# Kernel optimization log

Measured on AMD Instinct MI355X. Metric: run time of the kernel, lower is better.

Reference implementation:

```python
import jax, jax.numpy as jnp
import numpy as np

H = 4            # attention heads (HGTConv and SGFormer)
HID = 128        # hidden_dim
D = HID // H     # per-head dim in HGT
OUT = 128        # out_dim
L = 2            # number of HGT layers
NE, NA = 60000, 30000
E_EE, E_EA, E_AE = 150000, 75000, 75000


def setup_inputs() -> dict:
    ks = iter(jax.random.split(jax.random.key(0), 64))

    def nrm(shape, s=0.05):
        return jax.random.normal(next(ks), shape, dtype=jnp.float32) * s

    return {
        "x_entity": nrm((NE, HID), 1.0),
        "x_attr": nrm((NA, HID), 1.0),
        "Wkqv_ent": nrm((L, HID, 3 * HID)), "bkqv_ent": jnp.zeros((L, 3 * HID), jnp.float32),
        "Wkqv_att": nrm((L, HID, 3 * HID)), "bkqv_att": jnp.zeros((L, 3 * HID), jnp.float32),
        "Wout_ent": nrm((L, HID, HID)), "bout_ent": jnp.zeros((L, HID), jnp.float32),
        "Wout_att": nrm((L, HID, HID)), "bout_att": jnp.zeros((L, HID), jnp.float32),
        "skip_ent": jnp.ones((L,), jnp.float32), "skip_att": jnp.ones((L,), jnp.float32),
        "a_rel": nrm((L, 3, H, D, D), 0.1), "m_rel": nrm((L, 3, H, D, D), 0.1),
        "p_rel": jnp.ones((L, 3, H), jnp.float32),
        "ln_ent_g": jnp.ones((HID,), jnp.float32), "ln_ent_b": jnp.zeros((HID,), jnp.float32),
        "sg_fc_W": nrm((HID, HID)), "sg_fc_b": jnp.zeros((HID,), jnp.float32),
        "sg_ln0_g": jnp.ones((HID,), jnp.float32), "sg_ln0_b": jnp.zeros((HID,), jnp.float32),
        "sg_Wq": nrm((HID, HID * H)), "sg_bq": jnp.zeros((HID * H,), jnp.float32),
        "sg_Wk": nrm((HID, HID * H)), "sg_bk": jnp.zeros((HID * H,), jnp.float32),
        "sg_Wv": nrm((HID, HID * H)), "sg_bv": jnp.zeros((HID * H,), jnp.float32),
        "sg_ln1_g": jnp.ones((HID,), jnp.float32), "sg_ln1_b": jnp.zeros((HID,), jnp.float32),
        "proj_W1": nrm((HID, OUT)), "proj_b1": jnp.zeros((OUT,), jnp.float32),
        "proj_W2": nrm((OUT, OUT)), "proj_b2": jnp.zeros((OUT,), jnp.float32),
        "ei_ee": jax.random.randint(next(ks), (2, E_EE), 0, NE),
        "ei_ea": jnp.stack([jax.random.randint(next(ks), (E_EA,), 0, NE),
                            jax.random.randint(next(ks), (E_EA,), 0, NA)]),
        "ei_ae": jnp.stack([jax.random.randint(next(ks), (E_AE,), 0, NA),
                            jax.random.randint(next(ks), (E_AE,), 0, NE)]),
    }


def _ln(x, g, b, eps=1e-5):
    mu = x.mean(-1, keepdims=True)
    var = ((x - mu) ** 2).mean(-1, keepdims=True)
    return (x - mu) * jax.lax.rsqrt(var + eps) * g + b


def _seg_softmax(alpha, idx, n):
    # numerically stable softmax over edges grouped by destination node
    m = jax.ops.segment_max(alpha, idx, num_segments=n)
    e = jnp.exp(alpha - m[idx])
    s = jax.ops.segment_sum(e, idx, num_segments=n)
    return e / (s[idx] + 1e-16)


def _hgt_layer(x_e, x_a, Wkqv_e, bkqv_e, Wkqv_a, bkqv_a, Wout_e, bout_e,
               Wout_a, bout_a, sk_e, sk_a, a_rel, m_rel, p_rel,
               ei_ee, ei_ea, ei_ae):
    ne, na = x_e.shape[0], x_a.shape[0]
    # HeteroDictLinear producing [k|q|v], split along channels then reshape [N,H,D]
    kqv_e = (x_e @ Wkqv_e + bkqv_e).reshape(ne, 3, H, D)
    kqv_a = (x_a @ Wkqv_a + bkqv_a).reshape(na, 3, H, D)
    kd = {"e": kqv_e[:, 0], "a": kqv_a[:, 0]}
    qd = {"e": kqv_e[:, 1], "a": kqv_a[:, 1]}
    vd = {"e": kqv_e[:, 2], "a": kqv_a[:, 2]}
    nd = {"e": ne, "a": na}
    scale = 1.0 / float(np.sqrt(D))
    buf = {"e": [], "a": []}
    for t, (src, dst, ei) in enumerate([("e", "e", ei_ee), ("e", "a", ei_ea), ("a", "e", ei_ae)]):
        kt = jnp.einsum('nhd,hde->nhe', kd[src], a_rel[t])  # per-relation key transform (k_rel)
        vt = jnp.einsum('nhd,hde->nhe', vd[src], m_rel[t])  # per-relation value transform (v_rel)
        al = (qd[dst][ei[1]] * kt[ei[0]]).sum(-1) * p_rel[t] * scale  # [E,H]
        buf[dst].append((al, vt[ei[0]], ei[1]))
    outs = {}
    for dst in ("e", "a"):
        # joint softmax over ALL incoming edge types of this node type
        al = jnp.concatenate([b[0] for b in buf[dst]], 0)
        ve = jnp.concatenate([b[1] for b in buf[dst]], 0)
        ix = jnp.concatenate([b[2] for b in buf[dst]], 0)
        w = _seg_softmax(al, ix, nd[dst])
        outs[dst] = jax.ops.segment_sum(ve * w[..., None], ix,
                                        num_segments=nd[dst]).reshape(nd[dst], HID)
    o_e = jax.nn.gelu(outs["e"], approximate=False) @ Wout_e + bout_e
    o_a = jax.nn.gelu(outs["a"], approximate=False) @ Wout_a + bout_a
    g_e, g_a = jax.nn.sigmoid(sk_e), jax.nn.sigmoid(sk_a)
    return g_e * o_e + (1.0 - g_e) * x_e, g_a * o_a + (1.0 - g_a) * x_a


def reference(x_entity, x_attr, Wkqv_ent, bkqv_ent, Wkqv_att, bkqv_att,
              Wout_ent, bout_ent, Wout_att, bout_att, skip_ent, skip_att,
              a_rel, m_rel, p_rel, ln_ent_g, ln_ent_b,
              sg_fc_W, sg_fc_b, sg_ln0_g, sg_ln0_b, sg_Wq, sg_bq, sg_Wk, sg_bk,
              sg_Wv, sg_bv, sg_ln1_g, sg_ln1_b,
              proj_W1, proj_b1, proj_W2, proj_b2, ei_ee, ei_ea, ei_ae):
    h_e, h_a = x_entity, x_attr
    for l in range(L):
        h_e, h_a = _hgt_layer(h_e, h_a, Wkqv_ent[l], bkqv_ent[l], Wkqv_att[l], bkqv_att[l],
                              Wout_ent[l], bout_ent[l], Wout_att[l], bout_att[l],
                              skip_ent[l], skip_att[l], a_rel[l], m_rel[l], p_rel[l],
                              ei_ee, ei_ea, ei_ae)
        h_e = jax.nn.gelu(h_e, approximate=False)
        h_a = jax.nn.gelu(h_a, approximate=False)
    # SGFormer trans_conv: fc -> LN -> ReLU -> linear global attention -> residual -> LN
    n = h_e.shape[0]
    z0 = jax.nn.relu(_ln(h_e @ sg_fc_W + sg_fc_b, sg_ln0_g, sg_ln0_b))
    q = (z0 @ sg_Wq + sg_bq).reshape(n, H, HID)
    k = (z0 @ sg_Wk + sg_bk).reshape(n, H, HID)
    v = (z0 @ sg_Wv + sg_bv).reshape(n, H, HID)
    qs = q / jnp.linalg.norm(q)  # global Frobenius norm, as in SGFormer
    kn = k / jnp.linalg.norm(k)
    kvs = jnp.einsum('lhm,lhd->hmd', kn, v)
    num = jnp.einsum('nhm,hmd->nhd', qs, kvs) + float(n) * v
    den = jnp.einsum('nhm,hm->nh', qs, kn.sum(0))[..., None] + float(n)
    attn = (num / den).mean(1)  # mean over heads -> [n, HID]
    h_global = _ln(0.5 * attn + 0.5 * z0, sg_ln1_g, sg_ln1_b)  # residual alpha=0.5
    # alpha-blend (self.alpha = 0.1) + entity LayerNorm + projector MLP
    h_ent = _ln(0.9 * h_e + 0.1 * h_global, ln_ent_g, ln_ent_b)
    return jax.nn.relu(h_ent @ proj_W1 + proj_b1) @ proj_W2 + proj_b2
```

## Files before the change

### kernel.cpp

```cpp
#include <hip/hip_runtime.h>

#define NE 60000
#define NA 30000
#define E_EE 150000
#define E_EA 75000
#define E_AE 75000
#define SCALE 0.17677669529663689f

typedef __attribute__((ext_vector_type(8))) short bf16x8;
typedef __attribute__((ext_vector_type(4))) float f32x4;

__device__ __forceinline__ float bf2f(unsigned short u) {
  return __uint_as_float(((unsigned)u) << 16);
}
__device__ __forceinline__ unsigned short f2bf(float f) {
  unsigned u = __float_as_uint(f);
  u = u + 0x7FFFu + ((u >> 16) & 1u);
  return (unsigned short)(u >> 16);
}
__device__ __forceinline__ float ldc(const float* p) { return *p; }
__device__ __forceinline__ float ldc(const unsigned short* p) { return bf2f(*p); }
__device__ __forceinline__ float gelu_f(float x) {
  return 0.5f * x * (1.0f + erff(x * 0.7071067811865476f));
}

__global__ __launch_bounds__(256) void wrel_k(
    const float* __restrict__ Wk_e, const float* __restrict__ Wk_a,
    const float* __restrict__ bk_e, const float* __restrict__ bk_a,
    const float* __restrict__ a_rel, const float* __restrict__ m_rel,
    float* __restrict__ Wkt, float* __restrict__ Wvt,
    float* __restrict__ bkt, float* __restrict__ bvt) {
  int t = blockIdx.x;
  int part = blockIdx.y;
  const float* W = (t < 2) ? Wk_e : Wk_a;
  const float* bb = (t < 2) ? bk_e : bk_a;
  const float* A = (part ? m_rel : a_rel) + t * 4096;
  int coff = part ? 256 : 0;
  float* Wo = (part ? Wvt : Wkt) + t * 16384;
  float* bo = (part ? bvt : bkt) + t * 128;
  __shared__ float As[4096];
  for (int u = threadIdx.x; u < 4096; u += 256) As[u] = A[u];
  __syncthreads();
  for (int u = threadIdx.x; u < 16384; u += 256) {
    int i = u >> 7, c = u & 127;
    int hh = c >> 5, e = c & 31;
    const float* wr = W + i * 384 + coff + hh * 32;
    const float* ar = As + hh * 1024 + e;
    float acc = 0.f;
#pragma unroll
    for (int d = 0; d < 32; ++d) acc = fmaf(wr[d], ar[d * 32], acc);
    Wo[u] = acc;
  }
  if (threadIdx.x < 128) {
    int c = threadIdx.x, hh = c >> 5, e = c & 31;
    const float* br = bb + coff + hh * 32;
    const float* ar = As + hh * 1024 + e;
    float acc = 0.f;
#pragma unroll
    for (int d = 0; d < 32; ++d) acc = fmaf(br[d], ar[d * 32], acc);
    bo[c] = acc;
  }
}

template <int ACT, int EPI>
__global__ __launch_bounds__(256) void gemm128_k(
    const float* __restrict__ X, int ldx,
    const float* __restrict__ W, int ldw,
    const float* __restrict__ bias, int N,
    float* __restrict__ fout, unsigned short* __restrict__ bout, int ldo,
    const float* __restrict__ skipp, float* __restrict__ ssq) {
  __shared__ float Xs[128 * 32];
  __shared__ float Ws[32 * 128];
  const int tid = threadIdx.x;
  const int ti = tid >> 4;
  const int tj = tid & 15;
  const int row0 = blockIdx.x * 128;
  const int cb = blockIdx.y * 128;
  const int c0 = cb + tj * 4;
  const int c1 = cb + 64 + tj * 4;

  float acc[8][8];
  {
    float bc[8] = {0.f, 0.f, 0.f, 0.f, 0.f, 0.f, 0.f, 0.f};
    if (bias) {
#pragma unroll
      for (int j = 0; j < 4; ++j) { bc[j] = bias[c0 + j]; bc[4 + j] = bias[c1 + j]; }
    }
#pragma unroll
    for (int i = 0; i < 8; ++i)
#pragma unroll
      for (int j = 0; j < 8; ++j) acc[i][j] = bc[j];
  }

  for (int ks = 0; ks < 128; ks += 32) {
    __syncthreads();
    for (int v = tid; v < 1024; v += 256) {
      int kq = v & 7, r = v >> 3;
      int rg = row0 + r; if (rg >= N) rg = N - 1;
      float4 x4 = *reinterpret_cast<const float4*>(X + (size_t)rg * ldx + ks + kq * 4);
      if (ACT == 1) {
        x4.x = gelu_f(x4.x); x4.y = gelu_f(x4.y);
        x4.z = gelu_f(x4.z); x4.w = gelu_f(x4.w);
      }
      *reinterpret_cast<float4*>(&Xs[r * 32 + ((kq ^ ((r >> 3) & 7)) << 2)]) = x4;
    }
    for (int v = tid; v < 1024; v += 256) {
      int cq = v & 31, k = v >> 5;
      *reinterpret_cast<float4*>(&Ws[k * 128 + cq * 4]) =
          *reinterpret_cast<const float4*>(W + (size_t)(ks + k) * ldw + cb + cq * 4);
    }
    __syncthreads();
#pragma unroll
    for (int k = 0; k < 32; k += 4) {
      float xr[8][4];
#pragma unroll
      for (int i = 0; i < 8; ++i)
        *reinterpret_cast<float4*>(xr[i]) = *reinterpret_cast<const float4*>(
            &Xs[(ti * 8 + i) * 32 + ((((k >> 2)) ^ (ti & 7)) << 2)]);
      float wr[4][8];
#pragma unroll
      for (int dk = 0; dk < 4; ++dk) {
        *reinterpret_cast<float4*>(&wr[dk][0]) =
            *reinterpret_cast<const float4*>(&Ws[(k + dk) * 128 + tj * 4]);
        *reinterpret_cast<float4*>(&wr[dk][4]) =
            *reinterpret_cast<const float4*>(&Ws[(k + dk) * 128 + 64 + tj * 4]);
      }
#pragma unroll
      for (int i = 0; i < 8; ++i)
#pragma unroll
        for (int dk = 0; dk < 4; ++dk)
#pragma unroll
          for (int j = 0; j < 8; ++j)
            acc[i][j] = fmaf(xr[i][dk], wr[dk][j], acc[i][j]);
    }
  }

  if (EPI == 0 || EPI == 1) {
#pragma unroll
    for (int i = 0; i < 8; ++i) {
      int rg = row0 + ti * 8 + i;
      if (rg < N) {
        float4 a = make_float4(acc[i][0], acc[i][1], acc[i][2], acc[i][3]);
        float4 b = make_float4(acc[i][4], acc[i][5], acc[i][6], acc[i][7]);
        if (EPI == 1) {
          a.x = fmaxf(a.x, 0.f); a.y = fmaxf(a.y, 0.f);
          a.z = fmaxf(a.z, 0.f); a.w = fmaxf(a.w, 0.f);
          b.x = fmaxf(b.x, 0.f); b.y = fmaxf(b.y, 0.f);
          b.z = fmaxf(b.z, 0.f); b.w = fmaxf(b.w, 0.f);
        }
        *reinterpret_cast<float4*>(fout + (size_t)rg * ldo + c0) = a;
        *reinterpret_cast<float4*>(fout + (size_t)rg * ldo + c1) = b;
      }
    }
  } else if (EPI == 2) {
    float loc = 0.f;
#pragma unroll
    for (int i = 0; i < 8; ++i) {
      int rg = row0 + ti * 8 + i;
      if (rg < N) {
        ushort4 s0, s1;
        s0.x = f2bf(acc[i][0]); s0.y = f2bf(acc[i][1]);
        s0.z = f2bf(acc[i][2]); s0.w = f2bf(acc[i][3]);
        s1.x = f2bf(acc[i][4]); s1.y = f2bf(acc[i][5]);
        s1.z = f2bf(acc[i][6]); s1.w = f2bf(acc[i][7]);
        *reinterpret_cast<ushort4*>(bout + (size_t)rg * ldo + c0) = s0;
        *reinterpret_cast<ushort4*>(bout + (size_t)rg * ldo + c1) = s1;
#pragma unroll
        for (int j = 0; j < 8; ++j) loc += acc[i][j] * acc[i][j];
      }
    }
    if (ssq) {
      __syncthreads();
      Xs[tid] = loc;
      __syncthreads();
      if (tid < 128) Xs[tid] += Xs[tid + 128];
      __syncthreads();
      if (tid < 64) {
        float v = Xs[tid] + Xs[tid + 64];
#pragma unroll
        for (int m = 32; m > 0; m >>= 1) v += __shfl_down(v, m, 64);
        if (tid == 0) atomicAdd(ssq, v);
      }
    }
  } else {
    float g = 1.f / (1.f + expf(-*skipp));
    float g1 = 1.f - g;
#pragma unroll
    for (int i = 0; i < 8; ++i) {
      int rg = row0 + ti * 8 + i;
      if (rg < N) {
        float4 o0 = *reinterpret_cast<const float4*>(fout + (size_t)rg * ldo + c0);
        float4 o1 = *reinterpret_cast<const float4*>(fout + (size_t)rg * ldo + c1);
        float4 a, b;
        a.x = gelu_f(g * acc[i][0] + g1 * o0.x);
        a.y = gelu_f(g * acc[i][1] + g1 * o0.y);
        a.z = gelu_f(g * acc[i][2] + g1 * o0.z);
        a.w = gelu_f(g * acc[i][3] + g1 * o0.w);
        b.x = gelu_f(g * acc[i][4] + g1 * o1.x);
        b.y = gelu_f(g * acc[i][5] + g1 * o1.y);
        b.z = gelu_f(g * acc[i][6] + g1 * o1.z);
        b.w = gelu_f(g * acc[i][7] + g1 * o1.w);
        *reinterpret_cast<float4*>(fout + (size_t)rg * ldo + c0) = a;
        *reinterpret_cast<float4*>(fout + (size_t)rg * ldo + c1) = b;
      }
    }
  }
}

template <int ACT, int EPI>
__global__ __launch_bounds__(256) void gemm64_k(
    const float* __restrict__ X, int ldx,
    const float* __restrict__ W, int ldw,
    const float* __restrict__ bias, int N,
    float* __restrict__ fout, unsigned short* __restrict__ bout, int ldo,
    const float* __restrict__ skipp, float* __restrict__ ssq) {
  __shared__ float Xs[64 * 32];
  __shared__ float Ws[32 * 128];
  const int tid = threadIdx.x;
  const int ti = tid >> 4;
  const int tj = tid & 15;
  const int row0 = blockIdx.x * 64;
  const int cb = blockIdx.y * 128;
  const int c0 = cb + tj * 4;
  const int c1 = cb + 64 + tj * 4;

  float acc[4][8];
  {
    float bc[8] = {0.f, 0.f, 0.f, 0.f, 0.f, 0.f, 0.f, 0.f};
    if (bias) {
#pragma unroll
      for (int j = 0; j < 4; ++j) { bc[j] = bias[c0 + j]; bc[4 + j] = bias[c1 + j]; }
    }
#pragma unroll
    for (int i = 0; i < 4; ++i)
#pragma unroll
      for (int j = 0; j < 8; ++j) acc[i][j] = bc[j];
  }

  for (int ks = 0; ks < 128; ks += 32) {
    __syncthreads();
    for (int v = tid; v < 512; v += 256) {
      int kq = v & 7, r = v >> 3;
      int rg = row0 + r; if (rg >= N) rg = N - 1;
      float4 x4 = *reinterpret_cast<const float4*>(X + (size_t)rg * ldx + ks + kq * 4);
      if (ACT == 1) {
        x4.x = gelu_f(x4.x); x4.y = gelu_f(x4.y);
        x4.z = gelu_f(x4.z); x4.w = gelu_f(x4.w);
      }
      *reinterpret_cast<float4*>(&Xs[r * 32 + ((kq ^ ((r >> 3) & 7)) << 2)]) = x4;
    }
    for (int v = tid; v < 1024; v += 256) {
      int cq = v & 31, k = v >> 5;
      *reinterpret_cast<float4*>(&Ws[k * 128 + cq * 4]) =
          *reinterpret_cast<const float4*>(W + (size_t)(ks + k) * ldw + cb + cq * 4);
    }
    __syncthreads();
#pragma unroll
    for (int k = 0; k < 32; k += 4) {
      float xr[4][4];
#pragma unroll
      for (int i = 0; i < 4; ++i)
        *reinterpret_cast<float4*>(xr[i]) = *reinterpret_cast<const float4*>(
            &Xs[(ti * 4 + i) * 32 + ((((k >> 2)) ^ (ti >> 1)) << 2)]);
      float wr[4][8];
#pragma unroll
      for (int dk = 0; dk < 4; ++dk) {
        *reinterpret_cast<float4*>(&wr[dk][0]) =
            *reinterpret_cast<const float4*>(&Ws[(k + dk) * 128 + tj * 4]);
        *reinterpret_cast<float4*>(&wr[dk][4]) =
            *reinterpret_cast<const float4*>(&Ws[(k + dk) * 128 + 64 + tj * 4]);
      }
#pragma unroll
      for (int i = 0; i < 4; ++i)
#pragma unroll
        for (int dk = 0; dk < 4; ++dk)
#pragma unroll
          for (int j = 0; j < 8; ++j)
            acc[i][j] = fmaf(xr[i][dk], wr[dk][j], acc[i][j]);
    }
  }

  if (EPI == 0 || EPI == 1) {
#pragma unroll
    for (int i = 0; i < 4; ++i) {
      int rg = row0 + ti * 4 + i;
      if (rg < N) {
        float4 a = make_float4(acc[i][0], acc[i][1], acc[i][2], acc[i][3]);
        float4 b = make_float4(acc[i][4], acc[i][5], acc[i][6], acc[i][7]);
        if (EPI == 1) {
          a.x = fmaxf(a.x, 0.f); a.y = fmaxf(a.y, 0.f);
          a.z = fmaxf(a.z, 0.f); a.w = fmaxf(a.w, 0.f);
          b.x = fmaxf(b.x, 0.f); b.y = fmaxf(b.y, 0.f);
          b.z = fmaxf(b.z, 0.f); b.w = fmaxf(b.w, 0.f);
        }
        *reinterpret_cast<float4*>(fout + (size_t)rg * ldo + c0) = a;
        *reinterpret_cast<float4*>(fout + (size_t)rg * ldo + c1) = b;
      }
    }
  } else if (EPI == 2) {
    float loc = 0.f;
#pragma unroll
    for (int i = 0; i < 4; ++i) {
      int rg = row0 + ti * 4 + i;
      if (rg < N) {
        ushort4 s0, s1;
        s0.x = f2bf(acc[i][0]); s0.y = f2bf(acc[i][1]);
        s0.z = f2bf(acc[i][2]); s0.w = f2bf(acc[i][3]);
        s1.x = f2bf(acc[i][4]); s1.y = f2bf(acc[i][5]);
        s1.z = f2bf(acc[i][6]); s1.w = f2bf(acc[i][7]);
        *reinterpret_cast<ushort4*>(bout + (size_t)rg * ldo + c0) = s0;
        *reinterpret_cast<ushort4*>(bout + (size_t)rg * ldo + c1) = s1;
#pragma unroll
        for (int j = 0; j < 8; ++j) loc += acc[i][j] * acc[i][j];
      }
    }
    if (ssq) {
      __syncthreads();
      Xs[tid] = loc;
      __syncthreads();
      if (tid < 128) Xs[tid] += Xs[tid + 128];
      __syncthreads();
      if (tid < 64) {
        float v = Xs[tid] + Xs[tid + 64];
#pragma unroll
        for (int m = 32; m > 0; m >>= 1) v += __shfl_down(v, m, 64);
        if (tid == 0) atomicAdd(ssq, v);
      }
    }
  } else {
    float g = 1.f / (1.f + expf(-*skipp));
    float g1 = 1.f - g;
#pragma unroll
    for (int i = 0; i < 4; ++i) {
      int rg = row0 + ti * 4 + i;
      if (rg < N) {
        float4 o0 = *reinterpret_cast<const float4*>(fout + (size_t)rg * ldo + c0);
        float4 o1 = *reinterpret_cast<const float4*>(fout + (size_t)rg * ldo + c1);
        float4 a, b;
        a.x = gelu_f(g * acc[i][0] + g1 * o0.x);
        a.y = gelu_f(g * acc[i][1] + g1 * o0.y);
        a.z = gelu_f(g * acc[i][2] + g1 * o0.z);
        a.w = gelu_f(g * acc[i][3] + g1 * o0.w);
        b.x = gelu_f(g * acc[i][4] + g1 * o1.x);
        b.y = gelu_f(g * acc[i][5] + g1 * o1.y);
        b.z = gelu_f(g * acc[i][6] + g1 * o1.z);
        b.w = gelu_f(g * acc[i][7] + g1 * o1.w);
        *reinterpret_cast<float4*>(fout + (size_t)rg * ldo + c0) = a;
        *reinterpret_cast<float4*>(fout + (size_t)rg * ldo + c1) = b;
      }
    }
  }
}

template <int EPI>
__global__ __launch_bounds__(256) void gemmMF_k(
    const float* __restrict__ X, int ldx,
    const float* __restrict__ W, int ldw,
    const float* __restrict__ bias, int N,
    float* __restrict__ fout, unsigned short* __restrict__ bout, int ldo,
    float* __restrict__ ssq) {
  __shared__ short Bs[16384];
  const int tid = threadIdx.x;
  const int lane = tid & 63;
  const int w = tid >> 6;
  const int n0 = blockIdx.x * 64;
  const int cb = blockIdx.y * 128;

  for (int s = tid; s < 2048; s += 256) {
    int l = s & 63, dtks = s >> 6;
    int c = cb + (dtks >> 2) * 16 + (l & 15);
    int kk = (dtks & 3) * 32 + (l >> 4) * 8;
    bf16x8 b;
#pragma unroll
    for (int j = 0; j < 8; ++j)
      b[j] = (short)f2bf(W[(size_t)(kk + j) * ldw + c]);
    *reinterpret_cast<bf16x8*>(&Bs[s * 8]) = b;
  }

  int arow = n0 + w * 16 + (lane & 15);
  if (arow >= N) arow = N - 1;
  const int kofs = (lane >> 4) * 8;
  bf16x8 afr[4];
#pragma unroll
  for (int ks = 0; ks < 4; ++ks) {
    const float* xp = X + (size_t)arow * ldx + ks * 32 + kofs;
    float4 a0 = *reinterpret_cast<const float4*>(xp);
    float4 a1 = *reinterpret_cast<const float4*>(xp + 4);
    bf16x8 a;
    a[0] = (short)f2bf(a0.x); a[1] = (short)f2bf(a0.y);
    a[2] = (short)f2bf(a0.z); a[3] = (short)f2bf(a0.w);
    a[4] = (short)f2bf(a1.x); a[5] = (short)f2bf(a1.y);
    a[6] = (short)f2bf(a1.z); a[7] = (short)f2bf(a1.w);
    afr[ks] = a;
  }
  __syncthreads();

  float loc = 0.f;
#pragma unroll
  for (int dt = 0; dt < 8; ++dt) {
    f32x4 acc = {0.f, 0.f, 0.f, 0.f};
#pragma unroll
    for (int ks = 0; ks < 4; ++ks) {
      bf16x8 b = *reinterpret_cast<const bf16x8*>(&Bs[((dt * 4 + ks) * 64 + lane) * 8]);
      acc = __builtin_amdgcn_mfma_f32_16x16x32_bf16(afr[ks], b, acc, 0, 0, 0);
    }
    int dcol = dt * 16 + (lane & 15);
    float bv = bias ? bias[cb + dcol] : 0.f;
#pragma unroll
    for (int r = 0; r < 4; ++r) {
      int rg = n0 + w * 16 + (lane >> 4) * 4 + r;
      if (rg < N) {
        float val = acc[r] + bv;
        if (EPI == 0) {
          fout[(size_t)rg * ldo + cb + dcol] = val;
        } else {
          bout[(size_t)rg * ldo + cb + dcol] = f2bf(val);
          loc += val * val;
        }
      }
    }
  }
  if (EPI == 2 && ssq) {
    __syncthreads();
    float* red = (float*)Bs;
    red[tid] = loc;
    __syncthreads();
    if (tid < 128) red[tid] += red[tid + 128];
    __syncthreads();
    if (tid < 64) {
      float v = red[tid] + red[tid + 64];
#pragma unroll
      for (int m = 32; m > 0; m >>= 1) v += __shfl_down(v, m, 64);
      if (tid == 0) atomicAdd(ssq, v);
    }
  }
}

__global__ __launch_bounds__(256) void deg_k(const int* __restrict__ ei, int E,
                                             int* __restrict__ deg) {
  int i = blockIdx.x * 256 + threadIdx.x;
  if (i < E) atomicAdd(&deg[ei[E + i]], 1);
}

__global__ __launch_bounds__(1024) void scan_k(int* __restrict__ deg_cursor,
                                               int* __restrict__ rowptr, int n) {
  __shared__ int sd[1024];
  __shared__ int carry;
  int tid = threadIdx.x;
  if (tid == 0) carry = 0;
  __syncthreads();
  for (int base = 0; base < n; base += 1024) {
    int v = (base + tid < n) ? deg_cursor[base + tid] : 0;
    sd[tid] = v;
    __syncthreads();
    for (int off = 1; off < 1024; off <<= 1) {
      int t = (tid >= off) ? sd[tid - off] : 0;
      __syncthreads();
      sd[tid] += t;
      __syncthreads();
    }
    int c0 = carry;
    if (base + tid < n) {
      int excl = c0 + sd[tid] - v;
      rowptr[base + tid] = excl;
      deg_cursor[base + tid] = excl;
    }
    __syncthreads();
    if (tid == 0) carry = c0 + sd[1023];
    __syncthreads();
  }
  if (tid == 0) rowptr[n] = carry;
}

__global__ __launch_bounds__(256) void fill_k(const int* __restrict__ ei, int E,
                                              int* __restrict__ cursor,
                                              int* __restrict__ entries,
                                              int srcoff, int tag) {
  int i = blockIdx.x * 256 + threadIdx.x;
  if (i < E) {
    int pos = atomicAdd(&cursor[ei[E + i]], 1);
    entries[pos] = (ei[i] + srcoff) | (tag << 30);
  }
}

__global__ __launch_bounds__(256) void hgt_gather_k(
    const float* __restrict__ q, const unsigned short* __restrict__ ktbl,
    const unsigned short* __restrict__ vtbl, const int* __restrict__ rowptr,
    const int* __restrict__ entries, const float* __restrict__ pbase, int nd,
    float* __restrict__ out) {
  int g = blockIdx.x * 8 + (threadIdx.x >> 5);
  int dst = g >> 2, h = g & 3, c = threadIdx.x & 31;
  if (dst >= nd) return;
  int col = h * 32 + c;
  float qv = q[(size_t)dst * 128 + col];
  int i0 = rowptr[dst], i1 = rowptr[dst + 1];
  float sum = 0.f, acc = 0.f;
  for (int i = i0; i < i1; ++i) {
    int e = entries[i];
    int lin = e & 0x3FFFFFFF;
    int tag = (unsigned)e >> 30;
    float part = qv * bf2f(ktbl[(size_t)lin * 128 + col]);
#pragma unroll
    for (int m = 16; m > 0; m >>= 1) part += __shfl_xor(part, m);
    float w = expf(part * SCALE * pbase[tag * 8 + h]);
    sum += w;
    acc = fmaf(w, bf2f(vtbl[(size_t)lin * 128 + col]), acc);
  }
  out[(size_t)dst * 128 + col] = acc / (sum + 1e-16f);
}

template <typename AT, typename BT>
__global__ __launch_bounds__(128) void ln_k(const AT* __restrict__ A,
                                            const BT* __restrict__ B, float alpha,
                                            float beta, const float* __restrict__ g,
                                            const float* __restrict__ b,
                                            float* __restrict__ out, int relu) {
  int row = blockIdx.x;
  int t = threadIdx.x;
  float v = alpha * ldc(A + (size_t)row * 128 + t);
  if (B) v += beta * ldc(B + (size_t)row * 128 + t);
  float s1 = v, s2 = v * v;
#pragma unroll
  for (int m = 32; m > 0; m >>= 1) {
    s1 += __shfl_xor(s1, m, 64);
    s2 += __shfl_xor(s2, m, 64);
  }
  __shared__ float r1[2], r2[2];
  int w = t >> 6;
  if ((t & 63) == 0) { r1[w] = s1; r2[w] = s2; }
  __syncthreads();
  float S1 = r1[0] + r1[1], S2 = r2[0] + r2[1];
  float mu = S1 * (1.f / 128.f);
  float var = S2 * (1.f / 128.f) - mu * mu;
  float rr = rsqrtf(fmaxf(var, 0.f) + 1e-5f);
  float o = (v - mu) * rr * g[t] + b[t];
  if (relu) o = fmaxf(o, 0.f);
  out[(size_t)row * 128 + t] = o;
}

__global__ __launch_bounds__(256) void kvsred_k(const unsigned short* __restrict__ Kb,
                                                const unsigned short* __restrict__ Vb,
                                                float* __restrict__ part,
                                                float* __restrict__ ksum, int chunk) {
  const int h = blockIdx.y;
  const int n0 = blockIdx.x * chunk;
  const int iters = chunk >> 3;
  __shared__ float ks[8][132];
  __shared__ float vs[8][132];
  const int tid = threadIdx.x;
  const int ti = tid >> 4, tj = tid & 15;

  const int sw = tid >> 7;
  const int sni = (tid >> 4) & 7;
  const int sc = (tid & 15) << 3;
  const unsigned short* src =
      (sw ? Vb : Kb) + (size_t)(n0 + sni) * 512 + h * 128 + sc;
  float* dstrow = (sw ? &vs[0][0] : &ks[0][0]) + sni * 132 + sc;

  float acc[8][8];
#pragma unroll
  for (int i = 0; i < 8; ++i)
#pragma unroll
    for (int j = 0; j < 8; ++j) acc[i][j] = 0.f;
  float ksloc = 0.f;

  uint4 r = *reinterpret_cast<const uint4*>(src);
  for (int it = 0; it < iters; ++it) {
    __syncthreads();
    float4 lo, hi;
    lo.x = bf2f((unsigned short)(r.x & 0xffffu)); lo.y = bf2f((unsigned short)(r.x >> 16));
    lo.z = bf2f((unsigned short)(r.y & 0xffffu)); lo.w = bf2f((unsigned short)(r.y >> 16));
    hi.x = bf2f((unsigned short)(r.z & 0xffffu)); hi.y = bf2f((unsigned short)(r.z >> 16));
    hi.z = bf2f((unsigned short)(r.w & 0xffffu)); hi.w = bf2f((unsigned short)(r.w >> 16));
    *reinterpret_cast<float4*>(dstrow) = lo;
    *reinterpret_cast<float4*>(dstrow + 4) = hi;
    if (it + 1 < iters)
      r = *reinterpret_cast<const uint4*>(src + (size_t)(it + 1) * 8 * 512);
    __syncthreads();
#pragma unroll
    for (int ni = 0; ni < 8; ++ni) {
      float kk[8], vv[8];
      *reinterpret_cast<float4*>(kk) =
          *reinterpret_cast<const float4*>(&ks[ni][ti * 4]);
      *reinterpret_cast<float4*>(kk + 4) =
          *reinterpret_cast<const float4*>(&ks[ni][64 + ti * 4]);
      *reinterpret_cast<float4*>(vv) =
          *reinterpret_cast<const float4*>(&vs[ni][tj * 4]);
      *reinterpret_cast<float4*>(vv + 4) =
          *reinterpret_cast<const float4*>(&vs[ni][64 + tj * 4]);
#pragma unroll
      for (int i = 0; i < 8; ++i)
#pragma unroll
        for (int j = 0; j < 8; ++j) acc[i][j] = fmaf(kk[i], vv[j], acc[i][j]);
      if (tid < 128) ksloc += ks[ni][tid];
    }
  }
  float* pb = part + (size_t)(blockIdx.x * 4 + h) * 16384;
#pragma unroll
  for (int i = 0; i < 8; ++i) {
    int m = ti * 4 + (i & 3) + ((i >> 2) << 6);
    *reinterpret_cast<float4*>(pb + m * 128 + tj * 4) =
        make_float4(acc[i][0], acc[i][1], acc[i][2], acc[i][3]);
    *reinterpret_cast<float4*>(pb + m * 128 + 64 + tj * 4) =
        make_float4(acc[i][4], acc[i][5], acc[i][6], acc[i][7]);
  }
  if (tid < 128) atomicAdd(&ksum[h * 128 + tid], ksloc);
}

__global__ __launch_bounds__(256) void kvsfin_k(const float* __restrict__ part,
                                                float* __restrict__ kvs,
                                                unsigned short* __restrict__ kvsT,
                                                int G) {
  int c = blockIdx.x * 256 + threadIdx.x;
  int hh = c >> 14, md = c & 16383;
  int m = md >> 7, d = md & 127;
  const float* p = part + (size_t)hh * 16384 + md;
  float s = 0.f;
#pragma unroll 4
  for (int g = 0; g < G; ++g) s += p[(size_t)g * 65536];
  kvs[c] = s;
  kvsT[hh * 16384 + d * 128 + m] = f2bf(s);
}

__global__ __launch_bounds__(256) void sgapply_k(const unsigned short* __restrict__ Qb,
                                                 const unsigned short* __restrict__ Vb,
                                                 const unsigned short* __restrict__ kvsT,
                                                 const float* __restrict__ ksum,
                                                 const float* __restrict__ ssqq,
                                                 const float* __restrict__ ssqk,
                                                 unsigned short* __restrict__ attnb,
                                                 int N) {
  __shared__ short Bs[16384];
  __shared__ float den_s[64];
  __shared__ float fsh_s;
  const int tid = threadIdx.x;
  const int lane = tid & 63;
  const int w = tid >> 6;
  const int n0 = blockIdx.x * 64;
  if (tid == 0) fsh_s = 1.0f / (sqrtf(*ssqq) * sqrtf(*ssqk));

  float out[8][4];
#pragma unroll
  for (int dt = 0; dt < 8; ++dt)
#pragma unroll
    for (int r = 0; r < 4; ++r) out[dt][r] = 0.f;

  int arow = n0 + w * 16 + (lane & 15);
  if (arow >= N) arow = N - 1;
  const int kofs = (lane >> 4) * 8;

  for (int h = 0; h < 4; ++h) {
    __syncthreads();
    for (int s = tid; s < 2048; s += 256) {
      int l = s & 63, dtks = s >> 6;
      int d = (dtks >> 2) * 16 + (l & 15);
      int kk = (dtks & 3) * 32 + (l >> 4) * 8;
      *reinterpret_cast<bf16x8*>(&Bs[s * 8]) =
          *reinterpret_cast<const bf16x8*>(kvsT + h * 16384 + d * 128 + kk);
    }
    {
      int r = tid >> 2, seg = tid & 3;
      int rg = n0 + r; if (rg >= N) rg = N - 1;
      const unsigned short* qp = Qb + (size_t)rg * 512 + h * 128 + seg * 32;
      const float* kp = ksum + h * 128 + seg * 32;
      float p = 0.f;
#pragma unroll
      for (int u = 0; u < 32; u += 8) {
        bf16x8 q8 = *reinterpret_cast<const bf16x8*>(qp + u);
#pragma unroll
        for (int j = 0; j < 8; ++j)
          p = fmaf(bf2f((unsigned short)q8[j]), kp[u + j], p);
      }
      p += __shfl_xor(p, 1);
      p += __shfl_xor(p, 2);
      if (seg == 0) den_s[r] = p * fsh_s + 60000.0f;
    }
    __syncthreads();
    bf16x8 afr[4];
    {
      const unsigned short* qrow = Qb + (size_t)arow * 512 + h * 128 + kofs;
#pragma unroll
      for (int ks = 0; ks < 4; ++ks)
        afr[ks] = *reinterpret_cast<const bf16x8*>(qrow + ks * 32);
    }
    float f = fsh_s;
#pragma unroll
    for (int dt = 0; dt < 8; ++dt) {
      f32x4 acc = {0.f, 0.f, 0.f, 0.f};
#pragma unroll
      for (int ks = 0; ks < 4; ++ks) {
        bf16x8 b = *reinterpret_cast<const bf16x8*>(&Bs[((dt * 4 + ks) * 64 + lane) * 8]);
        acc = __builtin_amdgcn_mfma_f32_16x16x32_bf16(afr[ks], b, acc, 0, 0, 0);
      }
      int dcol = dt * 16 + (lane & 15);
#pragma unroll
      for (int r = 0; r < 4; ++r) {
        int rl = w * 16 + (lane >> 4) * 4 + r;
        int rg = n0 + rl;
        if (rg < N) {
          float v = bf2f(Vb[(size_t)rg * 512 + h * 128 + dcol]);
          float rd = 1.0f / den_s[rl];
          out[dt][r] += (acc[r] * f + 60000.0f * v) * rd;
        }
      }
    }
  }
#pragma unroll
  for (int dt = 0; dt < 8; ++dt) {
    int dcol = dt * 16 + (lane & 15);
#pragma unroll
    for (int r = 0; r < 4; ++r) {
      int rg = n0 + w * 16 + (lane >> 4) * 4 + r;
      if (rg < N) attnb[(size_t)rg * 128 + dcol] = f2bf(0.25f * out[dt][r]);
    }
  }
}

extern "C" void kernel_launch(void* const* d_in, const int* in_sizes, int n_in,
                              void* d_out, int out_size, void* d_ws, size_t ws_size,
                              hipStream_t stream) {
  const float* x_ent = (const float*)d_in[0];
  const float* x_att = (const float*)d_in[1];
  const float* Wkqv_e = (const float*)d_in[2];
  const float* bkqv_e = (const float*)d_in[3];
  const float* Wkqv_a = (const float*)d_in[4];
  const float* bkqv_a = (const float*)d_in[5];
  const float* Wout_e = (const float*)d_in[6];
  const float* bout_e = (const float*)d_in[7];
  const float* Wout_a = (const float*)d_in[8];
  const float* bout_a = (const float*)d_in[9];
  const float* skip_e = (const float*)d_in[10];
  const float* skip_a = (const float*)d_in[11];
  const float* a_rel = (const float*)d_in[12];
  const float* m_rel = (const float*)d_in[13];
  const float* p_rel = (const float*)d_in[14];
  const float* ln_ent_g = (const float*)d_in[15];
  const float* ln_ent_b = (const float*)d_in[16];
  const float* sg_fc_W = (const float*)d_in[17];
  const float* sg_fc_b = (const float*)d_in[18];
  const float* sg_ln0_g = (const float*)d_in[19];
  const float* sg_ln0_b = (const float*)d_in[20];
  const float* sg_Wq = (const float*)d_in[21];
  const float* sg_bq = (const float*)d_in[22];
  const float* sg_Wk = (const float*)d_in[23];
  const float* sg_bk = (const float*)d_in[24];
  const float* sg_Wv = (const float*)d_in[25];
  const float* sg_bv = (const float*)d_in[26];
  const float* sg_ln1_g = (const float*)d_in[27];
  const float* sg_ln1_b = (const float*)d_in[28];
  const float* proj_W1 = (const float*)d_in[29];
  const float* proj_b1 = (const float*)d_in[30];
  const float* proj_W2 = (const float*)d_in[31];
  const float* proj_b2 = (const float*)d_in[32];
  const int* ei_ee = (const int*)d_in[33];
  const int* ei_ea = (const int*)d_in[34];
  const int* ei_ae = (const int*)d_in[35];

  char* ws = (char*)d_ws;
  const size_t O_HE = 0;
  const size_t O_HA = 30720000;
  const size_t O_Z0 = 46080000;
  const size_t O_WKT = 76800000;
  const size_t O_WVT = 76996608;
  const size_t O_BKT = 77193216;
  const size_t O_BVT = 77194752;
  const size_t O_KVS = 77196288;
  const size_t O_RPE = 77460544;
  const size_t O_RPA = O_RPE + 240064;
  const size_t O_CUE = O_RPA + 120064;
  const size_t O_CUA = O_CUE + 240000;
  const size_t O_ENE = O_CUA + 120000;
  const size_t O_ENA = O_ENE + 900000;
  const size_t O_UN = O_ENA + 300000;
  float* q_e = (float*)(ws + O_UN);
  float* q_a = (float*)(ws + O_UN + 30720000);
  unsigned short* ktbl = (unsigned short*)(ws + O_UN + 46080000);
  unsigned short* vtbl = (unsigned short*)(ws + O_UN + 84480000);
  float* tmpf = (float*)(ws + O_UN);
  unsigned short* Vb = (unsigned short*)(ws + O_UN);
  unsigned short* KQb = (unsigned short*)(ws + O_UN + 61440000);
  unsigned short* attnb = (unsigned short*)(ws + O_HA);

  float* h_e = (float*)(ws + O_HE);
  float* h_a = (float*)(ws + O_HA);
  float* z0 = (float*)(ws + O_Z0);
  float* Wkt = (float*)(ws + O_WKT);
  float* Wvt = (float*)(ws + O_WVT);
  float* bkt = (float*)(ws + O_BKT);
  float* bvt = (float*)(ws + O_BVT);
  float* kvs = (float*)(ws + O_KVS);
  float* ksum = (float*)(ws + O_KVS + 262144);
  float* ssq_q = (float*)(ws + O_KVS + 262144 + 2048);
  float* ssq_k = ssq_q + 1;
  int* rowptr_e = (int*)(ws + O_RPE);
  int* rowptr_a = (int*)(ws + O_RPA);
  int* cursor_e = (int*)(ws + O_CUE);
  int* cursor_a = (int*)(ws + O_CUA);
  int* entries_e = (int*)(ws + O_ENE);
  int* entries_a = (int*)(ws + O_ENA);

  const int GB_E = (NE + 127) / 128;
  const int G64_E = (NE + 63) / 64;
  const int G64_A = (NA + 63) / 64;

  hipMemcpyAsync(h_e, x_ent, (size_t)NE * 128 * 4, hipMemcpyDeviceToDevice, stream);
  hipMemcpyAsync(h_a, x_att, (size_t)NA * 128 * 4, hipMemcpyDeviceToDevice, stream);

  hipMemsetAsync(ws + O_CUE, 0, 360000, stream);
  deg_k<<<(E_EE + 255) / 256, 256, 0, stream>>>(ei_ee, E_EE, cursor_e);
  deg_k<<<(E_AE + 255) / 256, 256, 0, stream>>>(ei_ae, E_AE, cursor_e);
  deg_k<<<(E_EA + 255) / 256, 256, 0, stream>>>(ei_ea, E_EA, cursor_a);
  scan_k<<<1, 1024, 0, stream>>>(cursor_e, rowptr_e, NE);
  scan_k<<<1, 1024, 0, stream>>>(cursor_a, rowptr_a, NA);
  fill_k<<<(E_EE + 255) / 256, 256, 0, stream>>>(ei_ee, E_EE, cursor_e, entries_e, 0, 0);
  fill_k<<<(E_AE + 255) / 256, 256, 0, stream>>>(ei_ae, E_AE, cursor_e, entries_e, NE, 1);
  fill_k<<<(E_EA + 255) / 256, 256, 0, stream>>>(ei_ea, E_EA, cursor_a, entries_a, 0, 0);

  for (int l = 0; l < 2; ++l) {
    const float* Wke = Wkqv_e + (size_t)l * 49152;
    const float* Wka = Wkqv_a + (size_t)l * 49152;
    const float* bke = bkqv_e + (size_t)l * 384;
    const float* bka = bkqv_a + (size_t)l * 384;

    wrel_k<<<dim3(3, 2), 256, 0, stream>>>(Wke, Wka, bke, bka,
                                           a_rel + (size_t)l * 12288,
                                           m_rel + (size_t)l * 12288, Wkt, Wvt, bkt, bvt);
    gemm64_k<0, 0><<<G64_E, 256, 0, stream>>>(h_e, 128, Wke + 128, 384, bke + 128, NE,
                                              q_e, nullptr, 128, nullptr, nullptr);
    gemm64_k<0, 0><<<G64_A, 256, 0, stream>>>(h_a, 128, Wka + 128, 384, bka + 128, NA,
                                              q_a, nullptr, 128, nullptr, nullptr);
    gemm64_k<0, 2><<<G64_E, 256, 0, stream>>>(h_e, 128, Wkt, 128, bkt, NE,
                                              nullptr, ktbl, 128, nullptr, nullptr);
    gemm64_k<0, 2><<<G64_A, 256, 0, stream>>>(h_a, 128, Wkt + 2 * 16384, 128,
                                              bkt + 2 * 128, NA, nullptr,
                                              ktbl + (size_t)NE * 128, 128, nullptr, nullptr);
    gemm64_k<0, 2><<<G64_E, 256, 0, stream>>>(h_e, 128, Wkt + 1 * 16384, 128,
                                              bkt + 1 * 128, NE, nullptr,
                                              ktbl + (size_t)90000 * 128, 128, nullptr, nullptr);
    gemm64_k<0, 2><<<G64_E, 256, 0, stream>>>(h_e, 128, Wvt, 128, bvt, NE,
                                              nullptr, vtbl, 128, nullptr, nullptr);
    gemm64_k<0, 2><<<G64_A, 256, 0, stream>>>(h_a, 128, Wvt + 2 * 16384, 128,
                                              bvt + 2 * 128, NA, nullptr,
                                              vtbl + (size_t)NE * 128, 128, nullptr, nullptr);
    gemm64_k<0, 2><<<G64_E, 256, 0, stream>>>(h_e, 128, Wvt + 1 * 16384, 128,
                                              bvt + 1 * 128, NE, nullptr,
                                              vtbl + (size_t)90000 * 128, 128, nullptr, nullptr);
    hgt_gather_k<<<30000, 256, 0, stream>>>(q_e, ktbl, vtbl, rowptr_e, entries_e,
                                            p_rel + (size_t)l * 12, NE, q_e);
    hgt_gather_k<<<15000, 256, 0, stream>>>(q_a, ktbl + (size_t)90000 * 128,
                                            vtbl + (size_t)90000 * 128, rowptr_a,
                                            entries_a, p_rel + (size_t)l * 12 + 4, NA, q_a);
    gemm64_k<1, 3><<<G64_E, 256, 0, stream>>>(q_e, 128, Wout_e + (size_t)l * 16384, 128,
                                              bout_e + (size_t)l * 128, NE, h_e, nullptr,
                                              128, skip_e + l, nullptr);
    gemm64_k<1, 3><<<G64_A, 256, 0, stream>>>(q_a, 128, Wout_a + (size_t)l * 16384, 128,
                                              bout_a + (size_t)l * 128, NA, h_a, nullptr,
                                              128, skip_a + l, nullptr);
  }

  gemmMF_k<0><<<dim3(G64_E, 1), 256, 0, stream>>>(h_e, 128, sg_fc_W, 128, sg_fc_b, NE,
                                                  tmpf, nullptr, 128, nullptr);
  ln_k<float, float><<<NE, 128, 0, stream>>>(tmpf, nullptr, 1.f, 0.f, sg_ln0_g,
                                             sg_ln0_b, z0, 1);
  hipMemsetAsync(ws + O_KVS, 0, 264256, stream);
  gemmMF_k<2><<<dim3(G64_E, 4), 256, 0, stream>>>(z0, 128, sg_Wv, 512, sg_bv, NE,
                                                  nullptr, Vb, 512, nullptr);
  gemmMF_k<2><<<dim3(G64_E, 4), 256, 0, stream>>>(z0, 128, sg_Wk, 512, sg_bk, NE,
                                                  nullptr, KQb, 512, ssq_k);
  unsigned short* kvsT = (unsigned short*)((char*)d_out + 26214400);
  kvsred_k<<<dim3(100, 4), 256, 0, stream>>>(KQb, Vb, (float*)d_out, ksum, 600);
  kvsfin_k<<<256, 256, 0, stream>>>((const float*)d_out, kvs, kvsT, 100);
  gemmMF_k<2><<<dim3(G64_E, 4), 256, 0, stream>>>(z0, 128, sg_Wq, 512, sg_bq, NE,
                                                  nullptr, KQb, 512, ssq_q);
  sgapply_k<<<G64_E, 256, 0, stream>>>(KQb, Vb, kvsT, ksum, ssq_q, ssq_k, attnb, NE);
  ln_k<unsigned short, float><<<NE, 128, 0, stream>>>(attnb, z0, 0.5f, 0.5f, sg_ln1_g,
                                                      sg_ln1_b, z0, 0);
  ln_k<float, float><<<NE, 128, 0, stream>>>(h_e, z0, 0.9f, 0.1f, ln_ent_g, ln_ent_b,
                                             h_e, 0);
  gemm64_k<0, 1><<<G64_E, 256, 0, stream>>>(h_e, 128, proj_W1, 128, proj_b1, NE,
                                            z0, nullptr, 128, nullptr, nullptr);
  gemm64_k<0, 0><<<G64_E, 256, 0, stream>>>(z0, 128, proj_W2, 128, proj_b2, NE,
                                            (float*)d_out, nullptr, 128, nullptr, nullptr);
}
```

Baseline: 1.825 ms.

## Compute SGFormer K^T V reduction with bf16 MFMA and split column sums

Rewrites the K^T·V partial reduction to use bf16 MFMA 16x16x32 instructions on an LDS tile laid out for the MFMA operands, replacing the scalar FMA outer-product loop. Partial results are now stored as bf16, which halves the traffic into the final reduce. The grid grows to 188 chunks of 320 rows with bounds checks. The K column sum moves into a separate colsum kernel that uses atomics. An unused 128-row GEMM kernel is deleted. Rounding the partial sums to bf16 adds precision loss in the global reduction.

```diff
diff --git a/kernel.cpp b/kernel.cpp
--- a/kernel.cpp
+++ b/kernel.cpp
@@ -63,151 +63,6 @@
 }
 
 template <int ACT, int EPI>
-__global__ __launch_bounds__(256) void gemm128_k(
-    const float* __restrict__ X, int ldx,
-    const float* __restrict__ W, int ldw,
-    const float* __restrict__ bias, int N,
-    float* __restrict__ fout, unsigned short* __restrict__ bout, int ldo,
-    const float* __restrict__ skipp, float* __restrict__ ssq) {
-  __shared__ float Xs[128 * 32];
-  __shared__ float Ws[32 * 128];
-  const int tid = threadIdx.x;
-  const int ti = tid >> 4;
-  const int tj = tid & 15;
-  const int row0 = blockIdx.x * 128;
-  const int cb = blockIdx.y * 128;
-  const int c0 = cb + tj * 4;
-  const int c1 = cb + 64 + tj * 4;
-
-  float acc[8][8];
-  {
-    float bc[8] = {0.f, 0.f, 0.f, 0.f, 0.f, 0.f, 0.f, 0.f};
-    if (bias) {
-#pragma unroll
-      for (int j = 0; j < 4; ++j) { bc[j] = bias[c0 + j]; bc[4 + j] = bias[c1 + j]; }
-    }
-#pragma unroll
-    for (int i = 0; i < 8; ++i)
-#pragma unroll
-      for (int j = 0; j < 8; ++j) acc[i][j] = bc[j];
-  }
-
-  for (int ks = 0; ks < 128; ks += 32) {
-    __syncthreads();
-    for (int v = tid; v < 1024; v += 256) {
-      int kq = v & 7, r = v >> 3;
-      int rg = row0 + r; if (rg >= N) rg = N - 1;
-      float4 x4 = *reinterpret_cast<const float4*>(X + (size_t)rg * ldx + ks + kq * 4);
-      if (ACT == 1) {
-        x4.x = gelu_f(x4.x); x4.y = gelu_f(x4.y);
-        x4.z = gelu_f(x4.z); x4.w = gelu_f(x4.w);
-      }
-      *reinterpret_cast<float4*>(&Xs[r * 32 + ((kq ^ ((r >> 3) & 7)) << 2)]) = x4;
-    }
-    for (int v = tid; v < 1024; v += 256) {
-      int cq = v & 31, k = v >> 5;
-      *reinterpret_cast<float4*>(&Ws[k * 128 + cq * 4]) =
-          *reinterpret_cast<const float4*>(W + (size_t)(ks + k) * ldw + cb + cq * 4);
-    }
-    __syncthreads();
-#pragma unroll
-    for (int k = 0; k < 32; k += 4) {
-      float xr[8][4];
-#pragma unroll
-      for (int i = 0; i < 8; ++i)
-        *reinterpret_cast<float4*>(xr[i]) = *reinterpret_cast<const float4*>(
-            &Xs[(ti * 8 + i) * 32 + ((((k >> 2)) ^ (ti & 7)) << 2)]);
-      float wr[4][8];
-#pragma unroll
-      for (int dk = 0; dk < 4; ++dk) {
-        *reinterpret_cast<float4*>(&wr[dk][0]) =
-            *reinterpret_cast<const float4*>(&Ws[(k + dk) * 128 + tj * 4]);
-        *reinterpret_cast<float4*>(&wr[dk][4]) =
-            *reinterpret_cast<const float4*>(&Ws[(k + dk) * 128 + 64 + tj * 4]);
-      }
-#pragma unroll
-      for (int i = 0; i < 8; ++i)
-#pragma unroll
-        for (int dk = 0; dk < 4; ++dk)
-#pragma unroll
-          for (int j = 0; j < 8; ++j)
-            acc[i][j] = fmaf(xr[i][dk], wr[dk][j], acc[i][j]);
-    }
-  }
-
-  if (EPI == 0 || EPI == 1) {
-#pragma unroll
-    for (int i = 0; i < 8; ++i) {
-      int rg = row0 + ti * 8 + i;
-      if (rg < N) {
-        float4 a = make_float4(acc[i][0], acc[i][1], acc[i][2], acc[i][3]);
-        float4 b = make_float4(acc[i][4], acc[i][5], acc[i][6], acc[i][7]);
-        if (EPI == 1) {
-          a.x = fmaxf(a.x, 0.f); a.y = fmaxf(a.y, 0.f);
-          a.z = fmaxf(a.z, 0.f); a.w = fmaxf(a.w, 0.f);
-          b.x = fmaxf(b.x, 0.f); b.y = fmaxf(b.y, 0.f);
-          b.z = fmaxf(b.z, 0.f); b.w = fmaxf(b.w, 0.f);
-        }
-        *reinterpret_cast<float4*>(fout + (size_t)rg * ldo + c0) = a;
-        *reinterpret_cast<float4*>(fout + (size_t)rg * ldo + c1) = b;
-      }
-    }
-  } else if (EPI == 2) {
-    float loc = 0.f;
-#pragma unroll
-    for (int i = 0; i < 8; ++i) {
-      int rg = row0 + ti * 8 + i;
-      if (rg < N) {
-        ushort4 s0, s1;
-        s0.x = f2bf(acc[i][0]); s0.y = f2bf(acc[i][1]);
-        s0.z = f2bf(acc[i][2]); s0.w = f2bf(acc[i][3]);
-        s1.x = f2bf(acc[i][4]); s1.y = f2bf(acc[i][5]);
-        s1.z = f2bf(acc[i][6]); s1.w = f2bf(acc[i][7]);
-        *reinterpret_cast<ushort4*>(bout + (size_t)rg * ldo + c0) = s0;
-        *reinterpret_cast<ushort4*>(bout + (size_t)rg * ldo + c1) = s1;
-#pragma unroll
-        for (int j = 0; j < 8; ++j) loc += acc[i][j] * acc[i][j];
-      }
-    }
-    if (ssq) {
-      __syncthreads();
-      Xs[tid] = loc;
-      __syncthreads();
-      if (tid < 128) Xs[tid] += Xs[tid + 128];
-      __syncthreads();
-      if (tid < 64) {
-        float v = Xs[tid] + Xs[tid + 64];
-#pragma unroll
-        for (int m = 32; m > 0; m >>= 1) v += __shfl_down(v, m, 64);
-        if (tid == 0) atomicAdd(ssq, v);
-      }
-    }
-  } else {
-    float g = 1.f / (1.f + expf(-*skipp));
-    float g1 = 1.f - g;
-#pragma unroll
-    for (int i = 0; i < 8; ++i) {
-      int rg = row0 + ti * 8 + i;
-      if (rg < N) {
-        float4 o0 = *reinterpret_cast<const float4*>(fout + (size_t)rg * ldo + c0);
-        float4 o1 = *reinterpret_cast<const float4*>(fout + (size_t)rg * ldo + c1);
-        float4 a, b;
-        a.x = gelu_f(g * acc[i][0] + g1 * o0.x);
-        a.y = gelu_f(g * acc[i][1] + g1 * o0.y);
-        a.z = gelu_f(g * acc[i][2] + g1 * o0.z);
-        a.w = gelu_f(g * acc[i][3] + g1 * o0.w);
-        b.x = gelu_f(g * acc[i][4] + g1 * o1.x);
-        b.y = gelu_f(g * acc[i][5] + g1 * o1.y);
-        b.z = gelu_f(g * acc[i][6] + g1 * o1.z);
-        b.w = gelu_f(g * acc[i][7] + g1 * o1.w);
-        *reinterpret_cast<float4*>(fout + (size_t)rg * ldo + c0) = a;
-        *reinterpret_cast<float4*>(fout + (size_t)rg * ldo + c1) = b;
-      }
-    }
-  }
-}
-
-template <int ACT, int EPI>
 __global__ __launch_bounds__(256) void gemm64_k(
     const float* __restrict__ X, int ldx,
     const float* __restrict__ W, int ldw,
@@ -538,86 +393,96 @@
   out[(size_t)row * 128 + t] = o;
 }
 
+__global__ __launch_bounds__(256) void colsum_k(const unsigned short* __restrict__ Kb,
+                                                float* __restrict__ ksum, int N) {
+  int c2 = threadIdx.x * 2;
+  int r0 = blockIdx.x * 128;
+  int r1 = r0 + 128; if (r1 > N) r1 = N;
+  float s0 = 0.f, s1 = 0.f;
+  for (int r = r0; r < r1; ++r) {
+    unsigned v = *reinterpret_cast<const unsigned*>(Kb + (size_t)r * 512 + c2);
+    s0 += bf2f((unsigned short)(v & 0xffffu));
+    s1 += bf2f((unsigned short)(v >> 16));
+  }
+  atomicAdd(&ksum[c2], s0);
+  atomicAdd(&ksum[c2 + 1], s1);
+}
+
 __global__ __launch_bounds__(256) void kvsred_k(const unsigned short* __restrict__ Kb,
                                                 const unsigned short* __restrict__ Vb,
-                                                float* __restrict__ part,
-                                                float* __restrict__ ksum, int chunk) {
+                                                unsigned short* __restrict__ part16,
+                                                int chunk, int N) {
+  __shared__ short Ks[4096];
+  __shared__ short Vs[4096];
+  const int tid = threadIdx.x;
+  const int lane = tid & 63;
+  const int w = tid >> 6;
   const int h = blockIdx.y;
-  const int n0 = blockIdx.x * chunk;
-  const int iters = chunk >> 3;
-  __shared__ float ks[8][132];
-  __shared__ float vs[8][132];
-  const int tid = threadIdx.x;
-  const int ti = tid >> 4, tj = tid & 15;
-
-  const int sw = tid >> 7;
-  const int sni = (tid >> 4) & 7;
-  const int sc = (tid & 15) << 3;
-  const unsigned short* src =
-      (sw ? Vb : Kb) + (size_t)(n0 + sni) * 512 + h * 128 + sc;
-  float* dstrow = (sw ? &vs[0][0] : &ks[0][0]) + sni * 132 + sc;
-
-  float acc[8][8];
-#pragma unroll
-  for (int i = 0; i < 8; ++i)
-#pragma unroll
-    for (int j = 0; j < 8; ++j) acc[i][j] = 0.f;
-  float ksloc = 0.f;
-
-  uint4 r = *reinterpret_cast<const uint4*>(src);
-  for (int it = 0; it < iters; ++it) {
-    __syncthreads();
-    float4 lo, hi;
-    lo.x = bf2f((unsigned short)(r.x & 0xffffu)); lo.y = bf2f((unsigned short)(r.x >> 16));
-    lo.z = bf2f((unsigned short)(r.y & 0xffffu)); lo.w = bf2f((unsigned short)(r.y >> 16));
-    hi.x = bf2f((unsigned short)(r.z & 0xffffu)); hi.y = bf2f((unsigned short)(r.z >> 16));
-    hi.z = bf2f((unsigned short)(r.w & 0xffffu)); hi.w = bf2f((unsigned short)(r.w >> 16));
-    *reinterpret_cast<float4*>(dstrow) = lo;
-    *reinterpret_cast<float4*>(dstrow + 4) = hi;
-    if (it + 1 < iters)
-      r = *reinterpret_cast<const uint4*>(src + (size_t)(it + 1) * 8 * 512);
-    __syncthreads();
-#pragma unroll
-    for (int ni = 0; ni < 8; ++ni) {
-      float kk[8], vv[8];
-      *reinterpret_cast<float4*>(kk) =
-          *reinterpret_cast<const float4*>(&ks[ni][ti * 4]);
-      *reinterpret_cast<float4*>(kk + 4) =
-          *reinterpret_cast<const float4*>(&ks[ni][64 + ti * 4]);
-      *reinterpret_cast<float4*>(vv) =
-          *reinterpret_cast<const float4*>(&vs[ni][tj * 4]);
-      *reinterpret_cast<float4*>(vv + 4) =
-          *reinterpret_cast<const float4*>(&vs[ni][64 + tj * 4]);
-#pragma unroll
-      for (int i = 0; i < 8; ++i)
-#pragma unroll
-        for (int j = 0; j < 8; ++j) acc[i][j] = fmaf(kk[i], vv[j], acc[i][j]);
-      if (tid < 128) ksloc += ks[ni][tid];
-    }
-  }
-  float* pb = part + (size_t)(blockIdx.x * 4 + h) * 16384;
-#pragma unroll
-  for (int i = 0; i < 8; ++i) {
-    int m = ti * 4 + (i & 3) + ((i >> 2) << 6);
-    *reinterpret_cast<float4*>(pb + m * 128 + tj * 4) =
-        make_float4(acc[i][0], acc[i][1], acc[i][2], acc[i][3]);
-    *reinterpret_cast<float4*>(pb + m * 128 + 64 + tj * 4) =
-        make_float4(acc[i][4], acc[i][5], acc[i][6], acc[i][7]);
-  }
-  if (tid < 128) atomicAdd(&ksum[h * 128 + tid], ksloc);
-}
-
-__global__ __launch_bounds__(256) void kvsfin_k(const float* __restrict__ part,
+  const int n0b = blockIdx.x * chunk;
+
+  f32x4 acc[2][8];
+#pragma unroll
+  for (int mi = 0; mi < 2; ++mi)
+#pragma unroll
+    for (int dt = 0; dt < 8; ++dt) acc[mi][dt] = (f32x4){0.f, 0.f, 0.f, 0.f};
+
+  for (int nc = 0; nc < chunk; nc += 32) {
+    int n0 = n0b + nc;
+    __syncthreads();
+    for (int u = tid; u < 1024; u += 256) {
+      int mat = u >> 9, rem = u & 511;
+      int nr = rem >> 4, c0 = (rem & 15) << 3;
+      int n = n0 + nr;
+      uint4 val = make_uint4(0u, 0u, 0u, 0u);
+      if (n < N)
+        val = *reinterpret_cast<const uint4*>(
+            (mat ? Vb : Kb) + (size_t)n * 512 + h * 128 + c0);
+      short* dst = mat ? Vs : Ks;
+      int base = (((c0 >> 4) * 64 + (nr >> 3) * 16 + (c0 & 15)) << 3) + (nr & 7);
+      unsigned short v[8];
+      v[0] = (unsigned short)(val.x & 0xffffu); v[1] = (unsigned short)(val.x >> 16);
+      v[2] = (unsigned short)(val.y & 0xffffu); v[3] = (unsigned short)(val.y >> 16);
+      v[4] = (unsigned short)(val.z & 0xffffu); v[5] = (unsigned short)(val.z >> 16);
+      v[6] = (unsigned short)(val.w & 0xffffu); v[7] = (unsigned short)(val.w >> 16);
+#pragma unroll
+      for (int i = 0; i < 8; ++i) dst[base + (i << 3)] = (short)v[i];
+    }
+    __syncthreads();
+    bf16x8 a0 = *reinterpret_cast<const bf16x8*>(&Ks[((2 * w) * 64 + lane) * 8]);
+    bf16x8 a1 = *reinterpret_cast<const bf16x8*>(&Ks[((2 * w + 1) * 64 + lane) * 8]);
+#pragma unroll
+    for (int dt = 0; dt < 8; ++dt) {
+      bf16x8 b = *reinterpret_cast<const bf16x8*>(&Vs[(dt * 64 + lane) * 8]);
+      acc[0][dt] = __builtin_amdgcn_mfma_f32_16x16x32_bf16(a0, b, acc[0][dt], 0, 0, 0);
+      acc[1][dt] = __builtin_amdgcn_mfma_f32_16x16x32_bf16(a1, b, acc[1][dt], 0, 0, 0);
+    }
+  }
+  unsigned short* pb = part16 + (size_t)(blockIdx.x * 4 + h) * 16384;
+#pragma unroll
+  for (int mi = 0; mi < 2; ++mi) {
+    int mt = 2 * w + mi;
+#pragma unroll
+    for (int dt = 0; dt < 8; ++dt) {
+      int col = dt * 16 + (lane & 15);
+#pragma unroll
+      for (int r = 0; r < 4; ++r) {
+        int row = mt * 16 + (lane >> 4) * 4 + r;
+        pb[row * 128 + col] = f2bf(acc[mi][dt][r]);
+      }
+    }
+  }
+}
+
+__global__ __launch_bounds__(256) void kvsfin_k(const unsigned short* __restrict__ part16,
                                                 float* __restrict__ kvs,
                                                 unsigned short* __restrict__ kvsT,
                                                 int G) {
   int c = blockIdx.x * 256 + threadIdx.x;
   int hh = c >> 14, md = c & 16383;
   int m = md >> 7, d = md & 127;
-  const float* p = part + (size_t)hh * 16384 + md;
   float s = 0.f;
-#pragma unroll 4
-  for (int g = 0; g < G; ++g) s += p[(size_t)g * 65536];
+  for (int g = 0; g < G; ++g)
+    s += bf2f(part16[((size_t)g * 4 + hh) * 16384 + md]);
   kvs[c] = s;
   kvsT[hh * 16384 + d * 128 + m] = f2bf(s);
 }
@@ -799,7 +664,6 @@
   int* entries_e = (int*)(ws + O_ENE);
   int* entries_a = (int*)(ws + O_ENA);
 
-  const int GB_E = (NE + 127) / 128;
   const int G64_E = (NE + 63) / 64;
   const int G64_A = (NA + 63) / 64;
 
@@ -867,9 +731,11 @@
                                                   nullptr, Vb, 512, nullptr);
   gemmMF_k<2><<<dim3(G64_E, 4), 256, 0, stream>>>(z0, 128, sg_Wk, 512, sg_bk, NE,
                                                   nullptr, KQb, 512, ssq_k);
-  unsigned short* kvsT = (unsigned short*)((char*)d_out + 26214400);
-  kvsred_k<<<dim3(100, 4), 256, 0, stream>>>(KQb, Vb, (float*)d_out, ksum, 600);
-  kvsfin_k<<<256, 256, 0, stream>>>((const float*)d_out, kvs, kvsT, 100);
+  colsum_k<<<469, 256, 0, stream>>>(KQb, ksum, NE);
+  unsigned short* part16 = (unsigned short*)d_out;
+  unsigned short* kvsT = (unsigned short*)((char*)d_out + 25000000);
+  kvsred_k<<<dim3(188, 4), 256, 0, stream>>>(KQb, Vb, part16, 320, NE);
+  kvsfin_k<<<256, 256, 0, stream>>>(part16, kvs, kvsT, 188);
   gemmMF_k<2><<<dim3(G64_E, 4), 256, 0, stream>>>(z0, 128, sg_Wq, 512, sg_bq, NE,
                                                   nullptr, KQb, 512, ssq_q);
   sgapply_k<<<G64_E, 256, 0, stream>>>(KQb, Vb, kvsT, ksum, ssq_q, ssq_k, attnb, NE);
```

After: 1.865 ms. 1.02x slower.
